# Kernel tuning notes

Hardware: AMD Instinct MI355X
Metric: run time of the kernel (lower is better)

The kernel has to match this reference:

```python
import jax, jax.numpy as jnp
import numpy as np

# The original module calls an opaque CPU extension (pixel_cluster_cpu.forward)
# performing offset-guided pixel grouping. This reference implements the
# standard vectorized semantics of such post-processing:
#  - valid pixels = non_zeros_map > 0 and pixel_gt > 0 (foreground instances)
#  - instance-balanced per-pixel weights: w = 1 / |instance| for valid pixels
#  - each pixel follows its predicted offset (dy, dx) to a target pixel; the
#    offset is 'correct' if the target belongs to the same gt instance
#  - pixel_weight  = w * sigmoid(pixel_pred)                  (B, R, C)
#  - offset_weight = (correct * w) * offset_pred              (B, 2, R, C)

MAX_INSTANCES = 16  # pixel_gt ids in [0, MAX_INSTANCES), 0 = background


def _cluster(non_zeros_map, pixel_pred, offset_pred, pixel_gt):
    B, R, C = pixel_gt.shape
    dt = pixel_pred.dtype
    mask = (non_zeros_map > 0) & (pixel_gt > 0)              # (B,R,C) bool
    maskf = mask.astype(dt)

    # instance sizes per batch element -> instance-balanced weights
    flat_gt = pixel_gt.reshape(B, -1)                        # (B, R*C)
    sizes = jax.vmap(
        lambda g, m: jax.ops.segment_sum(m, g, num_segments=MAX_INSTANCES)
    )(flat_gt, maskf.reshape(B, -1))                         # (B, MAX_INSTANCES)
    inv_size = 1.0 / jnp.maximum(sizes, 1.0)
    w = jnp.take_along_axis(inv_size, flat_gt, axis=1).reshape(B, R, C) * maskf

    # follow offsets: target pixel = round((r,c) + (dy,dx)), clipped to image
    rr = jnp.arange(R, dtype=dt)[:, None]                    # (R,1)
    cc = jnp.arange(C, dtype=dt)[None, :]                    # (1,C)
    ty = jnp.clip(jnp.round(rr + offset_pred[:, 0]), 0, R - 1).astype(jnp.int32)
    tx = jnp.clip(jnp.round(cc + offset_pred[:, 1]), 0, C - 1).astype(jnp.int32)
    gt_at_target = jax.vmap(lambda g, y, x: g[y, x])(pixel_gt, ty, tx)  # (B,R,C)
    agree = ((gt_at_target == pixel_gt) & mask).astype(dt)

    pixel_weight = w * jax.nn.sigmoid(pixel_pred)            # (B,R,C)
    offset_weight = (agree * w)[:, None] * offset_pred       # (B,2,R,C)
    return pixel_weight, offset_weight


def setup_inputs() -> dict:
    key = jax.random.key(0)
    k1, k2, k3, k4 = jax.random.split(key, 4)
    B, R, C = 8, 1024, 1024
    non_zeros_map = jax.random.randint(k1, (B, R, C), 0, 2).astype(jnp.int32)
    pixel_pred = jax.random.normal(k2, (B, R, C), dtype=jnp.float32)
    offset_pred = jax.random.normal(k3, (B, 2, R, C), dtype=jnp.float32) * 4.0
    pixel_gt = jax.random.randint(k4, (B, R, C), 0, MAX_INSTANCES).astype(jnp.int32)
    return {
        "non_zeros_map": non_zeros_map,
        "pixel_pred": pixel_pred,
        "offset_pred": offset_pred,
        "pixel_gt": pixel_gt,
    }


def reference(non_zeros_map, pixel_pred, offset_pred, pixel_gt):
    return _cluster(non_zeros_map, pixel_pred, offset_pred, pixel_gt)
```

## Files before the change

### kernel.cpp

```cpp
#include <hip/hip_runtime.h>
#include <cstdint>
#include <cstddef>

#define NB   8
#define RDIM 1024
#define CDIM 1024
#define PB   (RDIM * CDIM)
#define NI   16

__global__ __launch_bounds__(256) void count_pack_kernel(
    const int* __restrict__ nz, const int* __restrict__ gt,
    uint8_t* __restrict__ gt8, int* __restrict__ counts)
{
    __shared__ int s[68];
    const int b = blockIdx.y;
    for (int i = threadIdx.x; i < 68; i += blockDim.x) s[i] = 0;
    __syncthreads();

    const int rep = (threadIdx.x & 3) * 17;
    const int* nzb = nz + (size_t)b * PB;
    const int* gtb = gt + (size_t)b * PB;
    uint8_t* g8b = gt8 ? gt8 + (size_t)b * PB : nullptr;

    const int n4 = PB / 4;
    for (int i = blockIdx.x * blockDim.x + threadIdx.x; i < n4;
         i += gridDim.x * blockDim.x) {
        int4 nzv = ((const int4*)nzb)[i];
        int4 gv  = ((const int4*)gtb)[i];
        const int m0 = (nzv.x > 0) & (gv.x > 0);
        const int m1 = (nzv.y > 0) & (gv.y > 0);
        const int m2 = (nzv.z > 0) & (gv.z > 0);
        const int m3 = (nzv.w > 0) & (gv.w > 0);
        if (m0) atomicAdd(&s[rep + gv.x], 1);
        if (m1) atomicAdd(&s[rep + gv.y], 1);
        if (m2) atomicAdd(&s[rep + gv.z], 1);
        if (m3) atomicAdd(&s[rep + gv.w], 1);
        if (g8b) {
            uchar4 o;
            o.x = (uint8_t)(gv.x | (m0 << 7));
            o.y = (uint8_t)(gv.y | (m1 << 7));
            o.z = (uint8_t)(gv.z | (m2 << 7));
            o.w = (uint8_t)(gv.w | (m3 << 7));
            ((uchar4*)g8b)[i] = o;
        }
    }
    __syncthreads();
    if (threadIdx.x < NI) {
        int sum = s[threadIdx.x] + s[17 + threadIdx.x] +
                  s[34 + threadIdx.x] + s[51 + threadIdx.x];
        if (sum) atomicAdd(&counts[b * NI + threadIdx.x], sum);
    }
}

template <bool PACKED>
__global__ __launch_bounds__(256) void cluster_kernel(
    const float* __restrict__ pp, const float* __restrict__ op,
    const uint8_t* __restrict__ gt8,
    const int* __restrict__ nz, const int* __restrict__ gt,
    const int* __restrict__ counts, float* __restrict__ out)
{
    __shared__ float inv[NI];
    const int b = blockIdx.y;
    if (threadIdx.x < NI) {
        int c = counts[b * NI + threadIdx.x];
        inv[threadIdx.x] = 1.0f / (float)(c > 1 ? c : 1);
    }
    __syncthreads();

    const uint8_t* g8b = PACKED ? gt8 + (size_t)b * PB : nullptr;
    const int*     gtb = gt + (size_t)b * PB;
    const int*     nzb = nz + (size_t)b * PB;
    const float*   ppb = pp + (size_t)b * PB;
    const float*   dyb = op + (size_t)b * 2 * PB;
    const float*   dxb = dyb + PB;
    float* pwb  = out + (size_t)b * PB;
    float* owyb = out + (size_t)NB * PB + (size_t)b * 2 * PB;
    float* owxb = owyb + PB;

    const int n4 = PB / 4;
    for (int i = blockIdx.x * blockDim.x + threadIdx.x; i < n4;
         i += gridDim.x * blockDim.x) {
        const int p = i * 4;
        const float rf  = (float)(p >> 10);
        const float cf0 = (float)(p & (CDIM - 1));

        float4 ppv = ((const float4*)ppb)[i];
        float4 dyv = ((const float4*)dyb)[i];
        float4 dxv = ((const float4*)dxb)[i];

        int   gs[4];
        int   ms[4];
        if (PACKED) {
            uchar4 gv = ((const uchar4*)g8b)[i];
            const int raw[4] = {gv.x, gv.y, gv.z, gv.w};
            #pragma unroll
            for (int j = 0; j < 4; ++j) { gs[j] = raw[j] & 0x7f; ms[j] = raw[j] >> 7; }
        } else {
            int4 gv  = ((const int4*)gtb)[i];
            int4 nzv = ((const int4*)nzb)[i];
            const int g_[4] = {gv.x, gv.y, gv.z, gv.w};
            const int n_[4] = {nzv.x, nzv.y, nzv.z, nzv.w};
            #pragma unroll
            for (int j = 0; j < 4; ++j) { gs[j] = g_[j]; ms[j] = (n_[j] > 0) & (g_[j] > 0); }
        }

        const float pps[4] = {ppv.x, ppv.y, ppv.z, ppv.w};
        const float dys[4] = {dyv.x, dyv.y, dyv.z, dyv.w};
        const float dxs[4] = {dxv.x, dxv.y, dxv.z, dxv.w};
        float pw[4], oy[4], ox[4];

        #pragma unroll
        for (int j = 0; j < 4; ++j) {
            const float w = ms[j] ? inv[gs[j]] : 0.0f;
            float ty = fminf(fmaxf(rintf(rf + dys[j]), 0.0f), (float)(RDIM - 1));
            float tx = fminf(fmaxf(rintf(cf0 + (float)j + dxs[j]), 0.0f), (float)(CDIM - 1));
            const int ti = (int)ty * CDIM + (int)tx;
            int tg;
            if (PACKED) tg = g8b[ti] & 0x7f;
            else        tg = gtb[ti];
            const float aw = (ms[j] && (tg == gs[j])) ? w : 0.0f;
            pw[j] = w * (1.0f / (1.0f + __expf(-pps[j])));
            oy[j] = aw * dys[j];
            ox[j] = aw * dxs[j];
        }

        ((float4*)pwb)[i]  = make_float4(pw[0], pw[1], pw[2], pw[3]);
        ((float4*)owyb)[i] = make_float4(oy[0], oy[1], oy[2], oy[3]);
        ((float4*)owxb)[i] = make_float4(ox[0], ox[1], ox[2], ox[3]);
    }
}

extern "C" void kernel_launch(void* const* d_in, const int* in_sizes, int n_in,
                              void* d_out, int out_size, void* d_ws, size_t ws_size,
                              hipStream_t stream) {
    const int*   nz = (const int*)d_in[0];
    const float* pp = (const float*)d_in[1];
    const float* op = (const float*)d_in[2];
    const int*   gt = (const int*)d_in[3];
    float* out = (float*)d_out;

    int* counts = (int*)d_ws;
    const size_t need = 1024 + (size_t)NB * PB;
    const bool packed = ws_size >= need;
    uint8_t* gt8 = packed ? (uint8_t*)d_ws + 1024 : nullptr;

    hipMemsetAsync(counts, 0, NB * NI * sizeof(int), stream);

    dim3 blkA(256), grdA(512, NB);
    count_pack_kernel<<<grdA, blkA, 0, stream>>>(nz, gt, gt8, counts);

    dim3 blkB(256), grdB(1024, NB);
    if (packed)
        cluster_kernel<true><<<grdB, blkB, 0, stream>>>(pp, op, gt8, nz, gt, counts, out);
    else
        cluster_kernel<false><<<grdB, blkB, 0, stream>>>(pp, op, nullptr, nz, gt, counts, out);
}
```

Baseline: 241.2 us.

## Use ballot histograms, nontemporal memory ops, and swizzled one-shot cluster blocks

The count kernel replaces LDS atomics with wave-level ballot/popcount histograms accumulated in registers and halves its grid. The cluster kernel drops the grid-stride loop so each thread handles exactly one vector; block indices are swizzled across the row range and streaming loads and stores use nontemporal hints. The aim is to cut atomic contention and cache pollution. The cost is 60 ballots per iteration in the count kernel and a grid that must exactly cover the data.

Result: faster. 230.7 us (-4.4%).

```diff
diff --git a/kernel.cpp b/kernel.cpp
--- a/kernel.cpp
+++ b/kernel.cpp
@@ -8,47 +8,59 @@
 #define PB   (RDIM * CDIM)
 #define NI   16
 
+typedef int     i32x4 __attribute__((ext_vector_type(4)));
+typedef float   f32x4 __attribute__((ext_vector_type(4)));
+typedef uint8_t u8x4  __attribute__((ext_vector_type(4)));
+
 __global__ __launch_bounds__(256) void count_pack_kernel(
     const int* __restrict__ nz, const int* __restrict__ gt,
     uint8_t* __restrict__ gt8, int* __restrict__ counts)
 {
-    __shared__ int s[68];
-    const int b = blockIdx.y;
-    for (int i = threadIdx.x; i < 68; i += blockDim.x) s[i] = 0;
-    __syncthreads();
+    __shared__ unsigned s[4 * NI];
+    const int b    = blockIdx.y;
+    const int lane = threadIdx.x & 63;
+    const int wv   = threadIdx.x >> 6;
+    const i32x4* nzb = (const i32x4*)(nz + (size_t)b * PB);
+    const i32x4* gtb = (const i32x4*)(gt + (size_t)b * PB);
+    u8x4* g8b = gt8 ? (u8x4*)(gt8 + (size_t)b * PB) : nullptr;
 
-    const int rep = (threadIdx.x & 3) * 17;
-    const int* nzb = nz + (size_t)b * PB;
-    const int* gtb = gt + (size_t)b * PB;
-    uint8_t* g8b = gt8 ? gt8 + (size_t)b * PB : nullptr;
+    unsigned wc[NI];
+    #pragma unroll
+    for (int k = 0; k < NI; ++k) wc[k] = 0;
 
     const int n4 = PB / 4;
     for (int i = blockIdx.x * blockDim.x + threadIdx.x; i < n4;
          i += gridDim.x * blockDim.x) {
-        int4 nzv = ((const int4*)nzb)[i];
-        int4 gv  = ((const int4*)gtb)[i];
-        const int m0 = (nzv.x > 0) & (gv.x > 0);
-        const int m1 = (nzv.y > 0) & (gv.y > 0);
-        const int m2 = (nzv.z > 0) & (gv.z > 0);
-        const int m3 = (nzv.w > 0) & (gv.w > 0);
-        if (m0) atomicAdd(&s[rep + gv.x], 1);
-        if (m1) atomicAdd(&s[rep + gv.y], 1);
-        if (m2) atomicAdd(&s[rep + gv.z], 1);
-        if (m3) atomicAdd(&s[rep + gv.w], 1);
-        if (g8b) {
-            uchar4 o;
-            o.x = (uint8_t)(gv.x | (m0 << 7));
-            o.y = (uint8_t)(gv.y | (m1 << 7));
-            o.z = (uint8_t)(gv.z | (m2 << 7));
-            o.w = (uint8_t)(gv.w | (m3 << 7));
-            ((uchar4*)g8b)[i] = o;
+        i32x4 nzv = __builtin_nontemporal_load(&nzb[i]);
+        i32x4 gv  = __builtin_nontemporal_load(&gtb[i]);
+        int gm[4];
+        u8x4 o;
+        #pragma unroll
+        for (int j = 0; j < 4; ++j) {
+            const int g = gv[j];
+            const int m = (nzv[j] > 0) & (g > 0);
+            gm[j] = m ? g : 0;
+            o[j]  = (uint8_t)(g | (m << 7));
+        }
+        if (g8b) g8b[i] = o;
+        #pragma unroll
+        for (int j = 0; j < 4; ++j) {
+            #pragma unroll
+            for (int id = 1; id < NI; ++id) {
+                unsigned long long bal = __ballot(gm[j] == id);
+                wc[id] += (unsigned)__popcll(bal);
+            }
         }
     }
+    if (lane == 0) {
+        #pragma unroll
+        for (int id = 1; id < NI; ++id) s[wv * NI + id] = wc[id];
+    }
     __syncthreads();
-    if (threadIdx.x < NI) {
-        int sum = s[threadIdx.x] + s[17 + threadIdx.x] +
-                  s[34 + threadIdx.x] + s[51 + threadIdx.x];
-        if (sum) atomicAdd(&counts[b * NI + threadIdx.x], sum);
+    if (threadIdx.x >= 1 && threadIdx.x < NI) {
+        unsigned sum = s[threadIdx.x] + s[NI + threadIdx.x] +
+                       s[2 * NI + threadIdx.x] + s[3 * NI + threadIdx.x];
+        if (sum) atomicAdd((unsigned*)&counts[b * NI + threadIdx.x], sum);
     }
 }
 
@@ -67,6 +79,11 @@
     }
     __syncthreads();
 
+    const int nbx = gridDim.x;
+    const int p   = blockIdx.x;
+    const int bx  = (p & 7) * (nbx >> 3) + (p >> 3);
+    const int i   = bx * blockDim.x + threadIdx.x;
+
     const uint8_t* g8b = PACKED ? gt8 + (size_t)b * PB : nullptr;
     const int*     gtb = gt + (size_t)b * PB;
     const int*     nzb = nz + (size_t)b * PB;
@@ -77,57 +94,46 @@
     float* owyb = out + (size_t)NB * PB + (size_t)b * 2 * PB;
     float* owxb = owyb + PB;
 
-    const int n4 = PB / 4;
-    for (int i = blockIdx.x * blockDim.x + threadIdx.x; i < n4;
-         i += gridDim.x * blockDim.x) {
-        const int p = i * 4;
-        const float rf  = (float)(p >> 10);
-        const float cf0 = (float)(p & (CDIM - 1));
+    const int   pix = i * 4;
+    const float rf  = (float)(pix >> 10);
+    const float cf0 = (float)(pix & (CDIM - 1));
 
-        float4 ppv = ((const float4*)ppb)[i];
-        float4 dyv = ((const float4*)dyb)[i];
-        float4 dxv = ((const float4*)dxb)[i];
+    f32x4 ppv = __builtin_nontemporal_load((const f32x4*)ppb + i);
+    f32x4 dyv = __builtin_nontemporal_load((const f32x4*)dyb + i);
+    f32x4 dxv = __builtin_nontemporal_load((const f32x4*)dxb + i);
 
-        int   gs[4];
-        int   ms[4];
-        if (PACKED) {
-            uchar4 gv = ((const uchar4*)g8b)[i];
-            const int raw[4] = {gv.x, gv.y, gv.z, gv.w};
-            #pragma unroll
-            for (int j = 0; j < 4; ++j) { gs[j] = raw[j] & 0x7f; ms[j] = raw[j] >> 7; }
-        } else {
-            int4 gv  = ((const int4*)gtb)[i];
-            int4 nzv = ((const int4*)nzb)[i];
-            const int g_[4] = {gv.x, gv.y, gv.z, gv.w};
-            const int n_[4] = {nzv.x, nzv.y, nzv.z, nzv.w};
-            #pragma unroll
-            for (int j = 0; j < 4; ++j) { gs[j] = g_[j]; ms[j] = (n_[j] > 0) & (g_[j] > 0); }
-        }
+    int gs[4], ms[4];
+    if (PACKED) {
+        u8x4 gv = *((const u8x4*)g8b + i);
+        #pragma unroll
+        for (int j = 0; j < 4; ++j) { gs[j] = gv[j] & 0x7f; ms[j] = gv[j] >> 7; }
+    } else {
+        i32x4 gv  = *((const i32x4*)gtb + i);
+        i32x4 nzv = *((const i32x4*)nzb + i);
+        #pragma unroll
+        for (int j = 0; j < 4; ++j) { gs[j] = gv[j]; ms[j] = (nzv[j] > 0) & (gv[j] > 0); }
+    }
 
-        const float pps[4] = {ppv.x, ppv.y, ppv.z, ppv.w};
-        const float dys[4] = {dyv.x, dyv.y, dyv.z, dyv.w};
-        const float dxs[4] = {dxv.x, dxv.y, dxv.z, dxv.w};
-        float pw[4], oy[4], ox[4];
+    f32x4 pwv, oyv, oxv;
+    #pragma unroll
+    for (int j = 0; j < 4; ++j) {
+        const float dy = dyv[j], dx = dxv[j];
+        const float w  = ms[j] ? inv[gs[j]] : 0.0f;
+        float ty = fminf(fmaxf(rintf(rf + dy), 0.0f), (float)(RDIM - 1));
+        float tx = fminf(fmaxf(rintf(cf0 + (float)j + dx), 0.0f), (float)(CDIM - 1));
+        const int ti = (int)ty * CDIM + (int)tx;
+        int tg;
+        if (PACKED) tg = g8b[ti] & 0x7f;
+        else        tg = gtb[ti];
+        const float aw = (ms[j] && (tg == gs[j])) ? w : 0.0f;
+        pwv[j] = w * (1.0f / (1.0f + __expf(-ppv[j])));
+        oyv[j] = aw * dy;
+        oxv[j] = aw * dx;
+    }
 
-        #pragma unroll
-        for (int j = 0; j < 4; ++j) {
-            const float w = ms[j] ? inv[gs[j]] : 0.0f;
-            float ty = fminf(fmaxf(rintf(rf + dys[j]), 0.0f), (float)(RDIM - 1));
-            float tx = fminf(fmaxf(rintf(cf0 + (float)j + dxs[j]), 0.0f), (float)(CDIM - 1));
-            const int ti = (int)ty * CDIM + (int)tx;
-            int tg;
-            if (PACKED) tg = g8b[ti] & 0x7f;
-            else        tg = gtb[ti];
-            const float aw = (ms[j] && (tg == gs[j])) ? w : 0.0f;
-            pw[j] = w * (1.0f / (1.0f + __expf(-pps[j])));
-            oy[j] = aw * dys[j];
-            ox[j] = aw * dxs[j];
-        }
-
-        ((float4*)pwb)[i]  = make_float4(pw[0], pw[1], pw[2], pw[3]);
-        ((float4*)owyb)[i] = make_float4(oy[0], oy[1], oy[2], oy[3]);
-        ((float4*)owxb)[i] = make_float4(ox[0], ox[1], ox[2], ox[3]);
-    }
+    __builtin_nontemporal_store(pwv, (f32x4*)pwb  + i);
+    __builtin_nontemporal_store(oyv, (f32x4*)owyb + i);
+    __builtin_nontemporal_store(oxv, (f32x4*)owxb + i);
 }
 
 extern "C" void kernel_launch(void* const* d_in, const int* in_sizes, int n_in,
@@ -146,7 +152,7 @@
 
     hipMemsetAsync(counts, 0, NB * NI * sizeof(int), stream);
 
-    dim3 blkA(256), grdA(512, NB);
+    dim3 blkA(256), grdA(256, NB);
     count_pack_kernel<<<grdA, blkA, 0, stream>>>(nz, gt, gt8, counts);
 
     dim3 blkB(256), grdB(1024, NB);
```
